# Performance work log

Measured on AMD Instinct MI355X. Metric: run time of the kernel, lower is better.

The kernel has to match this reference:

```python
import jax, jax.numpy as jnp
import numpy as np
import math

B, S, V, E, H, MD, P, W = 2, 2048, 32000, 512, 1024, 256, 4096, 128

def setup_inputs() -> dict:
    key = jax.random.key(0)
    ks = jax.random.split(key, 24)
    sc = 0.02
    inp = {}
    inp['input_ids'] = jax.random.randint(ks[0], (B, S), 0, V)
    inp['untied_token_ids'] = jax.random.randint(ks[1], (P,), 0, V)
    inp['emb'] = jax.random.normal(ks[2], (V, E), jnp.float32) * sc
    inp['w_ih'] = jax.random.normal(ks[3], (3 * H, E), jnp.float32) * sc
    inp['w_hh'] = jax.random.normal(ks[4], (3 * H, H), jnp.float32) * sc
    inp['b_ih'] = jnp.zeros((3 * H,), jnp.float32)
    inp['b_hh'] = jnp.zeros((3 * H,), jnp.float32)
    inp['wq'] = jax.random.normal(ks[5], (MD, H), jnp.float32) * sc
    inp['bq'] = jnp.zeros((MD,), jnp.float32)
    inp['wk'] = jax.random.normal(ks[6], (MD, H), jnp.float32) * sc
    inp['bk'] = jnp.zeros((MD,), jnp.float32)
    inp['wv'] = jax.random.normal(ks[7], (E, H), jnp.float32) * sc
    inp['bv'] = jnp.zeros((E,), jnp.float32)
    inp['wg'] = jax.random.normal(ks[8], (1, H), jnp.float32) * sc
    inp['bg'] = jnp.zeros((1,), jnp.float32)
    inp['w_fc'] = jax.random.normal(ks[9], (4 * E, H), jnp.float32) * sc
    inp['b_fc'] = jnp.zeros((4 * E,), jnp.float32)
    inp['w_hp'] = jax.random.normal(ks[10], (E, 4 * E), jnp.float32) * sc
    inp['b_hp'] = jnp.zeros((E,), jnp.float32)
    inp['out_bias'] = jnp.zeros((V,), jnp.float32)
    inp['w_ph'] = jax.random.normal(ks[11], (P, E), jnp.float32) * sc
    inp['b_ph'] = jnp.zeros((P,), jnp.float32)
    inp['mem_scale'] = jnp.asarray(6.0, jnp.float32)
    return inp

def _gru(x, w_ih, w_hh, b_ih, b_hh):
    # x: [B,S,E] -> states [B,S,H]. Precompute input gates outside scan.
    gi = jnp.einsum('bse,ge->bsg', x, w_ih) + b_ih  # [B,S,3H]
    h0 = jnp.zeros((x.shape[0], w_hh.shape[1]), x.dtype)
    def step(h, gi_t):
        hg = h @ w_hh.T + b_hh
        gir, giz, gin = jnp.split(gi_t, 3, axis=-1)
        hgr, hgz, hgn = jnp.split(hg, 3, axis=-1)
        r = jax.nn.sigmoid(gir + hgr)
        z = jax.nn.sigmoid(giz + hgz)
        n = jnp.tanh(gin + r * hgn)
        h_new = (1.0 - z) * n + z * h
        return h_new, h_new
    _, hs = jax.lax.scan(step, h0, jnp.swapaxes(gi, 0, 1))  # [S,B,H]
    return jnp.swapaxes(hs, 0, 1)

def _forward(input_ids, untied_token_ids, emb, w_ih, w_hh, b_ih, b_hh, wq, bq,
             wk, bk, wv, bv, wg, bg, w_fc, b_fc, w_hp, b_hp, out_bias, w_ph,
             b_ph, mem_scale):
    x = emb[input_ids]                                   # [B,S,E]
    states = _gru(x, w_ih, w_hh, b_ih, b_hh)             # [B,S,H]
    hf = jnp.square(jax.nn.relu(states @ w_fc.T + b_fc)) # [B,S,4E]
    base_feat = hf @ w_hp.T + b_hp                       # [B,S,E]
    base_logits = base_feat @ emb.T + out_bias           # [B,S,V]
    base_partial = base_feat @ w_ph.T + b_ph             # [B,S,P]
    q = states @ wq.T + bq                               # [B,S,MD]
    k = states @ wk.T + bk
    v = states @ wv.T + bv                               # [B,S,E]
    scores = jnp.einsum('bqd,bkd->bqk', q, k) / math.sqrt(q.shape[-1])
    pos = jnp.arange(input_ids.shape[1])
    mask = (pos[None, :] < pos[:, None]) & (pos[None, :] >= pos[:, None] - W)
    neg = jnp.finfo(scores.dtype).min
    attn = jax.nn.softmax(jnp.where(mask[None], scores, neg), axis=-1)
    attn = attn * mask[None]
    attn = attn / jnp.clip(attn.sum(-1, keepdims=True), 1e-6)
    ctx = jnp.einsum('bqk,bke->bqe', attn, v)            # [B,S,E]
    gate = jax.nn.sigmoid(states @ wg.T + bg)            # [B,S,1]
    total_partial = base_partial + gate * mem_scale * (ctx @ w_ph.T + b_ph)
    return base_logits.at[:, :, untied_token_ids].add(total_partial)

def reference(input_ids, untied_token_ids, emb, w_ih, w_hh, b_ih, b_hh, wq,
              bq, wk, bk, wv, bv, wg, bg, w_fc, b_fc, w_hp, b_hp, out_bias,
              w_ph, b_ph, mem_scale):
    return _forward(input_ids, untied_token_ids, emb, w_ih, w_hh, b_ih, b_hh,
                    wq, bq, wk, bk, wv, bv, wg, bg, w_fc, b_fc, w_hp, b_hp,
                    out_bias, w_ph, b_ph, mem_scale)
```

## Files before the change

### kernel.cpp

```cpp
#include <hip/hip_runtime.h>
#include <math.h>

typedef __attribute__((ext_vector_type(4))) float f32x4;
typedef __attribute__((ext_vector_type(2))) float f32x2;
typedef __attribute__((ext_vector_type(8))) __bf16 bf16x8;
typedef __attribute__((ext_vector_type(4))) __bf16 bf16x4;
typedef __attribute__((ext_vector_type(4))) unsigned int u32x4;

#define DI __device__ __forceinline__

constexpr int Bd = 2, Sd = 2048, Vd = 32000, Ed = 512, Hd = 1024, MDd = 256, Pd = 4096, Wd = 128;
constexpr int BS = Bd * Sd;
constexpr int GBLK = 128;

DI float sigmoidf_(float x) { return 1.0f / (1.0f + expf(-x)); }

template<int EPI>
__global__ __launch_bounds__(256) void gemm_bt(
    const float* __restrict__ A, const float* __restrict__ Wt,
    const float* __restrict__ bias, float* __restrict__ C,
    int M, int N, int K, int ldc,
    const float* __restrict__ gate, const float* __restrict__ msp,
    const int* __restrict__ untied)
{
  __shared__ __bf16 As[128][40];
  __shared__ __bf16 Bs[128][40];
  const int tid  = threadIdx.x;
  const int lane = tid & 63, wv = tid >> 6;
  const int m0 = blockIdx.y * 128, n0 = blockIdx.x * 128;
  const int wrow = (wv >> 1) * 64, wcol = (wv & 1) * 64;

  f32x4 acc[4][4] = {};

  const int sr  = tid >> 3;
  const int sc4 = (tid & 7) << 2;
  const int nk  = K >> 5;

  for (int kt = 0; kt < nk; ++kt) {
    const int k0 = kt << 5;
    __syncthreads();
    #pragma unroll
    for (int i = 0; i < 4; ++i) {
      const int r = sr + 32 * i;
      f32x4 av = *reinterpret_cast<const f32x4*>(A  + (size_t)(m0 + r) * K + k0 + sc4);
      f32x4 bv = *reinterpret_cast<const f32x4*>(Wt + (size_t)(n0 + r) * K + k0 + sc4);
      bf16x4 ah, bh;
      ah.x = (__bf16)av.x; ah.y = (__bf16)av.y; ah.z = (__bf16)av.z; ah.w = (__bf16)av.w;
      bh.x = (__bf16)bv.x; bh.y = (__bf16)bv.y; bh.z = (__bf16)bv.z; bh.w = (__bf16)bv.w;
      *reinterpret_cast<bf16x4*>(&As[r][sc4]) = ah;
      *reinterpret_cast<bf16x4*>(&Bs[r][sc4]) = bh;
    }
    __syncthreads();

    bf16x8 af[4], bfr[4];
    #pragma unroll
    for (int t2 = 0; t2 < 4; ++t2) {
      af[t2]  = *reinterpret_cast<const bf16x8*>(&As[wrow + t2 * 16 + (lane & 15)][(lane >> 4) * 8]);
      bfr[t2] = *reinterpret_cast<const bf16x8*>(&Bs[wcol + t2 * 16 + (lane & 15)][(lane >> 4) * 8]);
    }
    #pragma unroll
    for (int mi = 0; mi < 4; ++mi)
      #pragma unroll
      for (int ni = 0; ni < 4; ++ni)
        acc[mi][ni] = __builtin_amdgcn_mfma_f32_16x16x32_bf16(af[mi], bfr[ni], acc[mi][ni], 0, 0, 0);
  }

  const float ms = (EPI == 3) ? msp[0] : 0.f;
  #pragma unroll
  for (int mi = 0; mi < 4; ++mi) {
    #pragma unroll
    for (int ni = 0; ni < 4; ++ni) {
      const int cc = n0 + wcol + ni * 16 + (lane & 15);
      const float bv = bias ? bias[cc] : 0.f;
      #pragma unroll
      for (int rg = 0; rg < 4; ++rg) {
        const int rr = m0 + wrow + mi * 16 + (lane >> 4) * 4 + rg;
        const float v = acc[mi][ni][rg];
        if (EPI == 0) {
          C[(size_t)rr * ldc + cc] = v + bv;
        } else if (EPI == 1) {
          float u = fmaxf(v + bv, 0.f);
          C[(size_t)rr * ldc + cc] = u * u;
        } else {
          float g = 1.f + gate[rr] * ms;
          atomicAdd(&C[(size_t)rr * ldc + untied[cc]], v + g * bv);
        }
      }
    }
  }
}

DI void poll2_coherent(const unsigned long long* p, u32x4& a) {
  asm volatile("global_load_dwordx4 %0, %1, off sc0 sc1\n\t"
               "s_waitcnt vmcnt(0)"
               : "=&v"(a) : "v"(p) : "memory");
}

__global__ __launch_bounds__(1024) void gru_kernel(
    const float* __restrict__ gi,
    const float* __restrict__ w_hh,
    const float* __restrict__ b_hh,
    float* __restrict__ states,
    unsigned long long* __restrict__ hb)
{
  __shared__ float hsm[Hd];
  __shared__ float gpre_sm[2][48];
  __shared__ float pubst[16];
  const int bid = blockIdx.x, tid = threadIdx.x;
  const int lane = tid & 63, wv = tid >> 6;
  const int b  = bid >> 6;
  const int gb = bid & 63;
  const int j  = gb * 16 + wv;

  f32x4 wr[4], wz[4], wn[4];
  #pragma unroll
  for (int c = 0; c < 4; ++c) {
    const int k = lane * 4 + c * 256;
    wr[c] = *reinterpret_cast<const f32x4*>(w_hh + (size_t)(0 * Hd + j) * Hd + k);
    wz[c] = *reinterpret_cast<const f32x4*>(w_hh + (size_t)(1 * Hd + j) * Hd + k);
    wn[c] = *reinterpret_cast<const f32x4*>(w_hh + (size_t)(2 * Hd + j) * Hd + k);
  }
  const float br = b_hh[j], bz = b_hh[Hd + j], bn = b_hh[2 * Hd + j];

  for (int i = tid; i < Hd; i += 1024) hsm[i] = 0.f;
  if (tid < 48) {
    const int g = tid >> 4, o = tid & 15;
    gpre_sm[0][tid] = gi[(size_t)b * Sd * 3 * Hd + g * Hd + gb * 16 + o];
  }
  __syncthreads();

  const int slot0 = (((tid & 511) + (gb << 3)) & 511) * 2;
  const bool poller = (tid < 512);

  for (int t = 0; t < Sd; ++t) {
    float d0 = 0, d1 = 0, d2 = 0;
    #pragma unroll
    for (int c = 0; c < 4; ++c) {
      f32x4 hv = *reinterpret_cast<const f32x4*>(&hsm[lane * 4 + c * 256]);
      d0 += wr[c].x*hv.x + wr[c].y*hv.y + wr[c].z*hv.z + wr[c].w*hv.w;
      d1 += wz[c].x*hv.x + wz[c].y*hv.y + wz[c].z*hv.z + wz[c].w*hv.w;
      d2 += wn[c].x*hv.x + wn[c].y*hv.y + wn[c].z*hv.z + wn[c].w*hv.w;
    }
    #pragma unroll
    for (int off = 32; off > 0; off >>= 1) {
      d0 += __shfl_xor(d0, off, 64);
      d1 += __shfl_xor(d1, off, 64);
      d2 += __shfl_xor(d2, off, 64);
    }

    const unsigned tagu = (unsigned)(t + 1);
    const unsigned long long tag = (unsigned long long)(t + 1);
    const int par = (t + 1) & 1;
    unsigned long long* hbp = hb + ((size_t)par * 2 + b) * Hd;

    const float pgr = gpre_sm[t & 1][wv];
    const float pgz = gpre_sm[t & 1][16 + wv];
    const float pgn = gpre_sm[t & 1][32 + wv];
    const float a  = (lane == 0) ? (pgr + d0 + br) : (pgz + d1 + bz);
    const float sg = sigmoidf_(a);
    const float r  = __shfl(sg, 0, 64);
    const float z  = __shfl(sg, 1, 64);
    const float n  = tanhf(pgn + r * (d2 + bn));
    const float ho = hsm[j];
    const float h  = (1.f - z) * n + z * ho;
    if (lane == 0) pubst[wv] = h;

    __syncthreads();

    if (tid < 16) {
      const float hv = pubst[tid];
      __hip_atomic_store(&hbp[gb * 16 + tid],
                         (tag << 32) | (unsigned long long)__float_as_uint(hv),
                         __ATOMIC_RELAXED, __HIP_MEMORY_SCOPE_AGENT);
    }

    if (tid >= 512 && tid < 560) {
      const int q = tid - 512;
      const int g = q >> 4, o = q & 15;
      const int tn = (t + 1 < Sd) ? (t + 1) : t;
      gpre_sm[par][q] = gi[((size_t)b * Sd + tn) * 3 * Hd + g * Hd + gb * 16 + o];
    }
    if (tid >= 576 && tid < 592) {
      const int q = tid - 576;
      states[((size_t)b * Sd + t) * Hd + gb * 16 + q] = pubst[q];
    }

    if (poller && t + 1 < Sd) {
      float v0 = 0, v1 = 0;
      bool done = false;
      for (int rounds = 0; rounds < 16384 && !done; ++rounds) {
        u32x4 a4;
        poll2_coherent(&hbp[slot0], a4);
        if (a4[1] == tagu && a4[3] == tagu) {
          v0 = __uint_as_float(a4[0]); v1 = __uint_as_float(a4[2]);
          done = true;
        } else if (rounds >= 6) {
          __builtin_amdgcn_s_sleep(1);
        }
      }
      if (!done) {
        bool f0 = false, f1 = false;
        do {
          unsigned long long x0, x1;
          if (!f0) x0 = __hip_atomic_load(&hbp[slot0 + 0], __ATOMIC_RELAXED, __HIP_MEMORY_SCOPE_AGENT);
          if (!f1) x1 = __hip_atomic_load(&hbp[slot0 + 1], __ATOMIC_RELAXED, __HIP_MEMORY_SCOPE_AGENT);
          if (!f0 && (x0 >> 32) == tag) { v0 = __uint_as_float((unsigned)x0); f0 = true; }
          if (!f1 && (x1 >> 32) == tag) { v1 = __uint_as_float((unsigned)x1); f1 = true; }
        } while (!(f0 && f1));
      }
      hsm[slot0]     = v0;
      hsm[slot0 + 1] = v1;
    }
    __syncthreads();
  }
}

__global__ __launch_bounds__(128) void embed_kernel(
    const int* __restrict__ ids, const float* __restrict__ emb, float* __restrict__ x)
{
  const int row = blockIdx.x;
  const int tok = ids[row];
  reinterpret_cast<f32x4*>(x)[(size_t)row * (Ed / 4) + threadIdx.x] =
      reinterpret_cast<const f32x4*>(emb)[(size_t)tok * (Ed / 4) + threadIdx.x];
}

__global__ __launch_bounds__(256) void gate_kernel(
    const float* __restrict__ states, const float* __restrict__ wg,
    const float* __restrict__ bg, float* __restrict__ gate)
{
  const int row = blockIdx.x * 4 + (threadIdx.x >> 6);
  const int lane = threadIdx.x & 63;
  float s = 0;
  for (int k = lane; k < Hd; k += 64) s += states[(size_t)row * Hd + k] * wg[k];
  #pragma unroll
  for (int off = 32; off > 0; off >>= 1) s += __shfl_down(s, off, 64);
  if (lane == 0) gate[row] = sigmoidf_(s + bg[0]);
}

__global__ __launch_bounds__(256) void attn_kernel(
    const float* __restrict__ q, const float* __restrict__ k,
    const float* __restrict__ v, float* __restrict__ featb,
    const float* __restrict__ gate, const float* __restrict__ msp)
{
  const int row = blockIdx.x;
  const int b = row >> 11, qi = row & (Sd - 1);
  const int tid = threadIdx.x, lane = tid & 63, wv = tid >> 6;
  __shared__ float qs[MDd];
  __shared__ float sc[Wd];
  qs[tid] = q[(size_t)row * MDd + tid];
  __syncthreads();
  const int lo = (qi > Wd) ? (qi - Wd) : 0;
  const int len = qi - lo;
  const float gm = gate[row] * msp[0];
  for (int jj = wv; jj < len; jj += 4) {
    const float* kr = k + (size_t)(b * Sd + lo + jj) * MDd;
    f32x4 kv = *reinterpret_cast<const f32x4*>(kr + lane * 4);
    f32x4 qv = *reinterpret_cast<const f32x4*>(&qs[lane * 4]);
    float s = kv.x * qv.x + kv.y * qv.y + kv.z * qv.z + kv.w * qv.w;
    #pragma unroll
    for (int off = 32; off > 0; off >>= 1) s += __shfl_down(s, off, 64);
    if (lane == 0) sc[jj] = s * 0.0625f;
  }
  __syncthreads();
  if (wv == 0 && len > 0) {
    float m = -3.4e38f;
    for (int jj = lane; jj < len; jj += 64) m = fmaxf(m, sc[jj]);
    #pragma unroll
    for (int off = 32; off > 0; off >>= 1) m = fmaxf(m, __shfl_xor(m, off, 64));
    float ssum = 0;
    for (int jj = lane; jj < len; jj += 64) { float e = expf(sc[jj] - m); sc[jj] = e; ssum += e; }
    #pragma unroll
    for (int off = 32; off > 0; off >>= 1) ssum += __shfl_xor(ssum, off, 64);
    const float inv = 1.f / ssum;
    for (int jj = lane; jj < len; jj += 64) sc[jj] *= inv;
  }
  __syncthreads();
  #pragma unroll
  for (int e0 = 0; e0 < Ed; e0 += 256) {
    const int e = e0 + tid;
    float a = 0;
    for (int jj = 0; jj < len; ++jj)
      a += sc[jj] * v[(size_t)(b * Sd + lo + jj) * Ed + e];
    featb[(size_t)row * Ed + e] += gm * a;
  }
}

extern "C" void kernel_launch(void* const* d_in, const int* in_sizes, int n_in,
                              void* d_out, int out_size, void* d_ws, size_t ws_size,
                              hipStream_t stream)
{
  const int*   ids    = (const int*)d_in[0];
  const int*   untied = (const int*)d_in[1];
  const float* emb    = (const float*)d_in[2];
  const float* w_ih   = (const float*)d_in[3];
  const float* w_hh   = (const float*)d_in[4];
  const float* b_ih   = (const float*)d_in[5];
  const float* b_hh   = (const float*)d_in[6];
  const float* wq     = (const float*)d_in[7];
  const float* bq     = (const float*)d_in[8];
  const float* wk     = (const float*)d_in[9];
  const float* bk     = (const float*)d_in[10];
  const float* wv     = (const float*)d_in[11];
  const float* bv     = (const float*)d_in[12];
  const float* wg     = (const float*)d_in[13];
  const float* bg     = (const float*)d_in[14];
  const float* w_fc   = (const float*)d_in[15];
  const float* b_fc   = (const float*)d_in[16];
  const float* w_hp   = (const float*)d_in[17];
  const float* b_hp   = (const float*)d_in[18];
  const float* out_b  = (const float*)d_in[19];
  const float* w_ph   = (const float*)d_in[20];
  const float* b_ph   = (const float*)d_in[21];
  const float* msc    = (const float*)d_in[22];
  float* out = (float*)d_out;

  float* ws      = (float*)d_ws;
  float* gi      = ws;
  float* states  = gi + (size_t)BS * 3 * Hd;
  float* featb   = states + (size_t)BS * Hd;
  float* hfb     = featb + (size_t)BS * Ed;
  unsigned long long* hb = (unsigned long long*)(hfb + (size_t)BS * 4 * Ed);

  float* qb    = hfb;
  float* kb    = qb + (size_t)BS * MDd;
  float* vb    = kb + (size_t)BS * MDd;
  float* gateb = vb + (size_t)BS * Ed;

  hipMemsetAsync(hb, 0, 2 * 2 * Hd * sizeof(unsigned long long), stream);

  embed_kernel<<<BS, 128, 0, stream>>>(ids, emb, featb);
  gemm_bt<0><<<dim3(3 * Hd / 128, BS / 128), 256, 0, stream>>>(
      featb, w_ih, b_ih, gi, BS, 3 * Hd, Ed, 3 * Hd, nullptr, nullptr, nullptr);
  gru_kernel<<<GBLK, 1024, 0, stream>>>(gi, w_hh, b_hh, states, hb);
  gemm_bt<1><<<dim3(4 * Ed / 128, BS / 128), 256, 0, stream>>>(
      states, w_fc, b_fc, hfb, BS, 4 * Ed, Hd, 4 * Ed, nullptr, nullptr, nullptr);
  gemm_bt<0><<<dim3(Ed / 128, BS / 128), 256, 0, stream>>>(
      hfb, w_hp, b_hp, featb, BS, Ed, 4 * Ed, Ed, nullptr, nullptr, nullptr);
  gemm_bt<0><<<dim3(Vd / 128, BS / 128), 256, 0, stream>>>(
      featb, emb, out_b, out, BS, Vd, Ed, Vd, nullptr, nullptr, nullptr);
  gemm_bt<0><<<dim3(MDd / 128, BS / 128), 256, 0, stream>>>(
      states, wq, bq, qb, BS, MDd, Hd, MDd, nullptr, nullptr, nullptr);
  gemm_bt<0><<<dim3(MDd / 128, BS / 128), 256, 0, stream>>>(
      states, wk, bk, kb, BS, MDd, Hd, MDd, nullptr, nullptr, nullptr);
  gemm_bt<0><<<dim3(Ed / 128, BS / 128), 256, 0, stream>>>(
      states, wv, bv, vb, BS, Ed, Hd, Ed, nullptr, nullptr, nullptr);
  gate_kernel<<<BS / 4, 256, 0, stream>>>(states, wg, bg, gateb);
  attn_kernel<<<BS, 256, 0, stream>>>(qb, kb, vb, featb, gateb, msc);
  gemm_bt<3><<<dim3(Pd / 128, BS / 128), 256, 0, stream>>>(
      featb, w_ph, b_ph, out, BS, Pd, Ed, Vd, gateb, msc, untied);
}
```

Baseline: 6.598 ms.

## Store activations and weights in bf16 and fuse Q/K/V projections into one GEMM

Weights are converted to bf16 once per call, and intermediate activations (states, hidden FC output, features) are written as bf16. The GEMM then loads bf16 directly with 8-wide vector loads instead of converting fp32 on every tile load. The Q, K and V projections become one GEMM over a concatenated weight, and the attention kernel writes a bf16 copy of its output for the final GEMM. This cuts memory traffic and per-tile conversion work, at the cost of extra conversion kernels per call and reduced precision in stored states.

```diff
diff --git a/kernel.cpp b/kernel.cpp
--- a/kernel.cpp
+++ b/kernel.cpp
@@ -16,9 +16,10 @@
 DI float sigmoidf_(float x) { return 1.0f / (1.0f + expf(-x)); }
 
 template<int EPI>
-__global__ __launch_bounds__(256) void gemm_bt(
-    const float* __restrict__ A, const float* __restrict__ Wt,
+__global__ __launch_bounds__(256) void gemm_h(
+    const __bf16* __restrict__ A, const __bf16* __restrict__ B,
     const float* __restrict__ bias, float* __restrict__ C,
+    __bf16* __restrict__ Ch,
     int M, int N, int K, int ldc,
     const float* __restrict__ gate, const float* __restrict__ msp,
     const int* __restrict__ untied)
@@ -32,23 +33,20 @@
 
   f32x4 acc[4][4] = {};
 
-  const int sr  = tid >> 3;
-  const int sc4 = (tid & 7) << 2;
+  const int sr  = tid >> 2;
+  const int sc8 = (tid & 3) * 8;
   const int nk  = K >> 5;
 
   for (int kt = 0; kt < nk; ++kt) {
     const int k0 = kt << 5;
     __syncthreads();
     #pragma unroll
-    for (int i = 0; i < 4; ++i) {
-      const int r = sr + 32 * i;
-      f32x4 av = *reinterpret_cast<const f32x4*>(A  + (size_t)(m0 + r) * K + k0 + sc4);
-      f32x4 bv = *reinterpret_cast<const f32x4*>(Wt + (size_t)(n0 + r) * K + k0 + sc4);
-      bf16x4 ah, bh;
-      ah.x = (__bf16)av.x; ah.y = (__bf16)av.y; ah.z = (__bf16)av.z; ah.w = (__bf16)av.w;
-      bh.x = (__bf16)bv.x; bh.y = (__bf16)bv.y; bh.z = (__bf16)bv.z; bh.w = (__bf16)bv.w;
-      *reinterpret_cast<bf16x4*>(&As[r][sc4]) = ah;
-      *reinterpret_cast<bf16x4*>(&Bs[r][sc4]) = bh;
+    for (int i = 0; i < 2; ++i) {
+      const int r = sr + 64 * i;
+      *reinterpret_cast<bf16x8*>(&As[r][sc8]) =
+          *reinterpret_cast<const bf16x8*>(A + (size_t)(m0 + r) * K + k0 + sc8);
+      *reinterpret_cast<bf16x8*>(&Bs[r][sc8]) =
+          *reinterpret_cast<const bf16x8*>(B + (size_t)(n0 + r) * K + k0 + sc8);
     }
     __syncthreads();
 
@@ -80,7 +78,11 @@
           C[(size_t)rr * ldc + cc] = v + bv;
         } else if (EPI == 1) {
           float u = fmaxf(v + bv, 0.f);
-          C[(size_t)rr * ldc + cc] = u * u;
+          Ch[(size_t)rr * ldc + cc] = (__bf16)(u * u);
+        } else if (EPI == 2) {
+          float o = v + bv;
+          C[(size_t)rr * ldc + cc] = o;
+          Ch[(size_t)rr * ldc + cc] = (__bf16)o;
         } else {
           float g = 1.f + gate[rr] * ms;
           atomicAdd(&C[(size_t)rr * ldc + untied[cc]], v + g * bv);
@@ -90,6 +92,19 @@
   }
 }
 
+__global__ __launch_bounds__(256) void convh(
+    const float* __restrict__ s, __bf16* __restrict__ d, int n)
+{
+  const int i = (blockIdx.x * 256 + threadIdx.x) * 8;
+  if (i >= n) return;
+  f32x4 a = *reinterpret_cast<const f32x4*>(s + i);
+  f32x4 b = *reinterpret_cast<const f32x4*>(s + i + 4);
+  bf16x8 o;
+  o[0] = (__bf16)a.x; o[1] = (__bf16)a.y; o[2] = (__bf16)a.z; o[3] = (__bf16)a.w;
+  o[4] = (__bf16)b.x; o[5] = (__bf16)b.y; o[6] = (__bf16)b.z; o[7] = (__bf16)b.w;
+  *reinterpret_cast<bf16x8*>(d + i) = o;
+}
+
 DI void poll2_coherent(const unsigned long long* p, u32x4& a) {
   asm volatile("global_load_dwordx4 %0, %1, off sc0 sc1\n\t"
                "s_waitcnt vmcnt(0)"
@@ -100,7 +115,7 @@
     const float* __restrict__ gi,
     const float* __restrict__ w_hh,
     const float* __restrict__ b_hh,
-    float* __restrict__ states,
+    __bf16* __restrict__ statesh,
     unsigned long long* __restrict__ hb)
 {
   __shared__ float hsm[Hd];
@@ -182,7 +197,7 @@
     }
     if (tid >= 576 && tid < 592) {
       const int q = tid - 576;
-      states[((size_t)b * Sd + t) * Hd + gb * 16 + q] = pubst[q];
+      statesh[((size_t)b * Sd + t) * Hd + gb * 16 + q] = (__bf16)pubst[q];
     }
 
     if (poller && t + 1 < Sd) {
@@ -216,30 +231,37 @@
 }
 
 __global__ __launch_bounds__(128) void embed_kernel(
-    const int* __restrict__ ids, const float* __restrict__ emb, float* __restrict__ x)
+    const int* __restrict__ ids, const float* __restrict__ emb, __bf16* __restrict__ xh)
 {
   const int row = blockIdx.x;
   const int tok = ids[row];
-  reinterpret_cast<f32x4*>(x)[(size_t)row * (Ed / 4) + threadIdx.x] =
-      reinterpret_cast<const f32x4*>(emb)[(size_t)tok * (Ed / 4) + threadIdx.x];
+  f32x4 v = reinterpret_cast<const f32x4*>(emb + (size_t)tok * Ed)[threadIdx.x];
+  bf16x4 o;
+  o[0] = (__bf16)v.x; o[1] = (__bf16)v.y; o[2] = (__bf16)v.z; o[3] = (__bf16)v.w;
+  reinterpret_cast<bf16x4*>(xh + (size_t)row * Ed)[threadIdx.x] = o;
 }
 
 __global__ __launch_bounds__(256) void gate_kernel(
-    const float* __restrict__ states, const float* __restrict__ wg,
+    const __bf16* __restrict__ statesh, const float* __restrict__ wg,
     const float* __restrict__ bg, float* __restrict__ gate)
 {
   const int row = blockIdx.x * 4 + (threadIdx.x >> 6);
   const int lane = threadIdx.x & 63;
+  const __bf16* sp = statesh + (size_t)row * Hd + lane * 16;
+  bf16x8 a0 = *reinterpret_cast<const bf16x8*>(sp);
+  bf16x8 a1 = *reinterpret_cast<const bf16x8*>(sp + 8);
   float s = 0;
-  for (int k = lane; k < Hd; k += 64) s += states[(size_t)row * Hd + k] * wg[k];
+  #pragma unroll
+  for (int i = 0; i < 8; ++i)
+    s += (float)a0[i] * wg[lane * 16 + i] + (float)a1[i] * wg[lane * 16 + 8 + i];
   #pragma unroll
   for (int off = 32; off > 0; off >>= 1) s += __shfl_down(s, off, 64);
   if (lane == 0) gate[row] = sigmoidf_(s + bg[0]);
 }
 
 __global__ __launch_bounds__(256) void attn_kernel(
-    const float* __restrict__ q, const float* __restrict__ k,
-    const float* __restrict__ v, float* __restrict__ featb,
+    const float* __restrict__ qkv, const float* __restrict__ featb,
+    __bf16* __restrict__ ffh,
     const float* __restrict__ gate, const float* __restrict__ msp)
 {
   const int row = blockIdx.x;
@@ -247,13 +269,13 @@
   const int tid = threadIdx.x, lane = tid & 63, wv = tid >> 6;
   __shared__ float qs[MDd];
   __shared__ float sc[Wd];
-  qs[tid] = q[(size_t)row * MDd + tid];
+  qs[tid] = qkv[(size_t)row * 1024 + tid];
   __syncthreads();
   const int lo = (qi > Wd) ? (qi - Wd) : 0;
   const int len = qi - lo;
   const float gm = gate[row] * msp[0];
   for (int jj = wv; jj < len; jj += 4) {
-    const float* kr = k + (size_t)(b * Sd + lo + jj) * MDd;
+    const float* kr = qkv + (size_t)(b * Sd + lo + jj) * 1024 + 256;
     f32x4 kv = *reinterpret_cast<const f32x4*>(kr + lane * 4);
     f32x4 qv = *reinterpret_cast<const f32x4*>(&qs[lane * 4]);
     float s = kv.x * qv.x + kv.y * qv.y + kv.z * qv.z + kv.w * qv.w;
@@ -280,8 +302,8 @@
     const int e = e0 + tid;
     float a = 0;
     for (int jj = 0; jj < len; ++jj)
-      a += sc[jj] * v[(size_t)(b * Sd + lo + jj) * Ed + e];
-    featb[(size_t)row * Ed + e] += gm * a;
+      a += sc[jj] * qkv[(size_t)(b * Sd + lo + jj) * 1024 + 512 + e];
+    ffh[(size_t)row * Ed + e] = (__bf16)(featb[(size_t)row * Ed + e] + gm * a);
   }
 }
 
@@ -314,38 +336,58 @@
   const float* msc    = (const float*)d_in[22];
   float* out = (float*)d_out;
 
-  float* ws      = (float*)d_ws;
-  float* gi      = ws;
-  float* states  = gi + (size_t)BS * 3 * Hd;
-  float* featb   = states + (size_t)BS * Hd;
-  float* hfb     = featb + (size_t)BS * Ed;
-  unsigned long long* hb = (unsigned long long*)(hfb + (size_t)BS * 4 * Ed);
-
-  float* qb    = hfb;
-  float* kb    = qb + (size_t)BS * MDd;
-  float* vb    = kb + (size_t)BS * MDd;
-  float* gateb = vb + (size_t)BS * Ed;
+  char* W = (char*)d_ws;
+  size_t off = 0;
+  auto nxt = [&](size_t bytes) { char* p = W + off; off += (bytes + 255) & ~(size_t)255; return p; };
+  float*  gi      = (float*) nxt((size_t)BS * 3 * Hd * 4);
+  __bf16* statesh = (__bf16*)nxt((size_t)BS * Hd * 2);
+  float*  featb   = (float*) nxt((size_t)BS * Ed * 4);
+  __bf16* embh    = (__bf16*)nxt((size_t)Vd * Ed * 2);
+  __bf16* wih_h   = (__bf16*)nxt((size_t)3 * Hd * Ed * 2);
+  __bf16* wfc_h   = (__bf16*)nxt((size_t)4 * Ed * Hd * 2);
+  __bf16* whp_h   = (__bf16*)nxt((size_t)Ed * 4 * Ed * 2);
+  __bf16* wqkv_h  = (__bf16*)nxt((size_t)1024 * Hd * 2);
+  __bf16* wph_h   = (__bf16*)nxt((size_t)Pd * Ed * 2);
+  __bf16* xh      = (__bf16*)nxt((size_t)BS * Ed * 2);
+  float*  bqkv    = (float*) nxt(1024 * 4);
+  unsigned long long* hb = (unsigned long long*)nxt(2 * 2 * Hd * 8);
+  float*  gateb   = (float*) nxt((size_t)BS * 4);
+  __bf16* hfh    = (__bf16*)gi;
+  __bf16* feat_h = (__bf16*)((char*)gi + 16777216);
+  __bf16* ffh    = (__bf16*)((char*)gi + 20971520);
+  float*  qkv    = (float*) ((char*)gi + 25165824);
 
   hipMemsetAsync(hb, 0, 2 * 2 * Hd * sizeof(unsigned long long), stream);
 
-  embed_kernel<<<BS, 128, 0, stream>>>(ids, emb, featb);
-  gemm_bt<0><<<dim3(3 * Hd / 128, BS / 128), 256, 0, stream>>>(
-      featb, w_ih, b_ih, gi, BS, 3 * Hd, Ed, 3 * Hd, nullptr, nullptr, nullptr);
-  gru_kernel<<<GBLK, 1024, 0, stream>>>(gi, w_hh, b_hh, states, hb);
-  gemm_bt<1><<<dim3(4 * Ed / 128, BS / 128), 256, 0, stream>>>(
-      states, w_fc, b_fc, hfb, BS, 4 * Ed, Hd, 4 * Ed, nullptr, nullptr, nullptr);
-  gemm_bt<0><<<dim3(Ed / 128, BS / 128), 256, 0, stream>>>(
-      hfb, w_hp, b_hp, featb, BS, Ed, 4 * Ed, Ed, nullptr, nullptr, nullptr);
-  gemm_bt<0><<<dim3(Vd / 128, BS / 128), 256, 0, stream>>>(
-      featb, emb, out_b, out, BS, Vd, Ed, Vd, nullptr, nullptr, nullptr);
-  gemm_bt<0><<<dim3(MDd / 128, BS / 128), 256, 0, stream>>>(
-      states, wq, bq, qb, BS, MDd, Hd, MDd, nullptr, nullptr, nullptr);
-  gemm_bt<0><<<dim3(MDd / 128, BS / 128), 256, 0, stream>>>(
-      states, wk, bk, kb, BS, MDd, Hd, MDd, nullptr, nullptr, nullptr);
-  gemm_bt<0><<<dim3(Ed / 128, BS / 128), 256, 0, stream>>>(
-      states, wv, bv, vb, BS, Ed, Hd, Ed, nullptr, nullptr, nullptr);
-  gate_kernel<<<BS / 4, 256, 0, stream>>>(states, wg, bg, gateb);
-  attn_kernel<<<BS, 256, 0, stream>>>(qb, kb, vb, featb, gateb, msc);
-  gemm_bt<3><<<dim3(Pd / 128, BS / 128), 256, 0, stream>>>(
-      featb, w_ph, b_ph, out, BS, Pd, Ed, Vd, gateb, msc, untied);
-}
+  auto cv = [&](const float* s, __bf16* d, size_t n) {
+    convh<<<(int)((n / 8 + 255) / 256), 256, 0, stream>>>(s, d, (int)n);
+  };
+  cv(emb,  embh,  (size_t)Vd * Ed);
+  cv(w_ih, wih_h, (size_t)3 * Hd * Ed);
+  cv(w_fc, wfc_h, (size_t)4 * Ed * Hd);
+  cv(w_hp, whp_h, (size_t)Ed * 4 * Ed);
+  cv(wq,   wqkv_h,                 (size_t)MDd * Hd);
+  cv(wk,   wqkv_h + (size_t)MDd * Hd,  (size_t)MDd * Hd);
+  cv(wv,   wqkv_h + (size_t)512 * Hd,  (size_t)Ed * Hd);
+  cv(w_ph, wph_h, (size_t)Pd * Ed);
+  hipMemcpyAsync(bqkv,       bq, MDd * 4, hipMemcpyDeviceToDevice, stream);
+  hipMemcpyAsync(bqkv + MDd, bk, MDd * 4, hipMemcpyDeviceToDevice, stream);
+  hipMemcpyAsync(bqkv + 512, bv, Ed * 4,  hipMemcpyDeviceToDevice, stream);
+
+  embed_kernel<<<BS, 128, 0, stream>>>(ids, emb, xh);
+  gemm_h<0><<<dim3(3 * Hd / 128, BS / 128), 256, 0, stream>>>(
+      xh, wih_h, b_ih, gi, nullptr, BS, 3 * Hd, Ed, 3 * Hd, nullptr, nullptr, nullptr);
+  gru_kernel<<<GBLK, 1024, 0, stream>>>(gi, w_hh, b_hh, statesh, hb);
+  gemm_h<1><<<dim3(4 * Ed / 128, BS / 128), 256, 0, stream>>>(
+      statesh, wfc_h, b_fc, nullptr, hfh, BS, 4 * Ed, Hd, 4 * Ed, nullptr, nullptr, nullptr);
+  gemm_h<2><<<dim3(Ed / 128, BS / 128), 256, 0, stream>>>(
+      hfh, whp_h, b_hp, featb, feat_h, BS, Ed, 4 * Ed, Ed, nullptr, nullptr, nullptr);
+  gemm_h<0><<<dim3(Vd / 128, BS / 128), 256, 0, stream>>>(
+      feat_h, embh, out_b, out, nullptr, BS, Vd, Ed, Vd, nullptr, nullptr, nullptr);
+  gemm_h<0><<<dim3(1024 / 128, BS / 128), 256, 0, stream>>>(
+      statesh, wqkv_h, bqkv, qkv, nullptr, BS, 1024, Hd, 1024, nullptr, nullptr, nullptr);
+  gate_kernel<<<BS / 4, 256, 0, stream>>>(statesh, wg, bg, gateb);
+  attn_kernel<<<BS, 256, 0, stream>>>(qkv, featb, ffh, gateb, msc);
+  gemm_h<3><<<dim3(Pd / 128, BS / 128), 256, 0, stream>>>(
+      ffh, wph_h, b_ph, out, nullptr, BS, Pd, Ed, Vd, gateb, msc, untied);
+}
```

New measurement: 6.417 ms. 2.7% less time.
